# Kernel tuning notes

Measured on AMD Instinct MI355X. Metric: run time of the kernel, lower is better.

The kernel has to match this reference:

```python
import jax, jax.numpy as jnp
import numpy as np

N, D, H = 1024, 256, 512


def _linear_init(key, fan_in, fan_out):
    kw, kb = jax.random.split(key)
    bound = 1.0 / np.sqrt(fan_in)
    w = jax.random.uniform(kw, (fan_in, fan_out), jnp.float32, -bound, bound)
    b = jax.random.uniform(kb, (fan_out,), jnp.float32, -bound, bound)
    return w, b


def setup_inputs() -> dict:
    key = jax.random.key(0)
    ks = jax.random.split(key, 8)
    domain_a = jax.random.normal(ks[0], (N, D), jnp.float32)
    domain_b = jax.random.normal(ks[1], (N, D), jnp.float32)
    mu_w0, mu_b0 = _linear_init(ks[2], D, H)
    mu_w1, mu_b1 = _linear_init(ks[3], H, H)
    mu_w2, mu_b2 = _linear_init(ks[4], H, D)
    lv_w0, lv_b0 = _linear_init(ks[5], D, H)
    lv_w1, lv_b1 = _linear_init(ks[6], H, H)
    lv_w2, lv_b2 = _linear_init(ks[7], H, D)
    return dict(domain_a=domain_a, domain_b=domain_b,
                mu_w0=mu_w0, mu_b0=mu_b0, mu_w1=mu_w1, mu_b1=mu_b1, mu_w2=mu_w2, mu_b2=mu_b2,
                lv_w0=lv_w0, lv_b0=lv_b0, lv_w1=lv_w1, lv_b1=lv_b1, lv_w2=lv_w2, lv_b2=lv_b2)


def _net(x, ws, bs, final_act):
    h = x
    for i in range(len(ws)):
        h = h @ ws[i] + bs[i]
        if i < len(ws) - 1:
            h = jax.nn.relu(h)
    return final_act(h)


def _l2norm(h):
    # L2NormEncoder == F.normalize(dim=-1), eps clamp like torch
    n = jnp.maximum(jnp.linalg.norm(h, axis=-1, keepdims=True), 1e-12)
    return h / n


def reference(domain_a, domain_b, mu_w0, mu_b0, mu_w1, mu_b1, mu_w2, mu_b2,
              lv_w0, lv_b0, lv_w1, lv_b1, lv_w2, lv_b2):
    mu_ws, mu_bs = [mu_w0, mu_w1, mu_w2], [mu_b0, mu_b1, mu_b2]
    lv_ws, lv_bs = [lv_w0, lv_w1, lv_w2], [lv_b0, lv_b1, lv_b2]

    # ---- embedding-model loss: prob-model params frozen (requires_grad=False) ----
    sg = jax.lax.stop_gradient
    mu = _net(domain_a, [sg(w) for w in mu_ws], [sg(b) for b in mu_bs], _l2norm)
    log_var = _net(domain_a, [sg(w) for w in lv_ws], [sg(b) for b in lv_bs], jnp.tanh)
    inv_var = jnp.exp(-log_var)                                  # [N, D]
    pos_probs = jnp.sum(-(domain_b - mu) ** 2 * inv_var - log_var, axis=-1)  # [N]
    # pairwise: [i, j, d] = b[j, d] - mu[i, d]; mean over j
    diff2_mean = jnp.mean((domain_b[None, :, :] - mu[:, None, :]) ** 2, axis=1)  # [N, D]
    neg_probs = jnp.sum(-diff2_mean * inv_var - log_var, axis=-1)  # [N]
    embed_model_loss = jnp.mean(pos_probs - neg_probs)

    # ---- prob-model loss: embeddings detached, params trainable ----
    a_d, b_d = sg(domain_a), sg(domain_b)
    mu2 = _net(a_d, mu_ws, mu_bs, _l2norm)
    lv2 = _net(a_d, lv_ws, lv_bs, jnp.tanh)
    prob_model_loss = jnp.mean(jnp.sum((b_d - mu2) ** 2 * jnp.exp(-lv2) + lv2, axis=-1))

    emb_coef, prob_coef = 1.0, 1.0
    loss = emb_coef * embed_model_loss + prob_coef * prob_model_loss
    return loss
```

## Files before the change

kernel.cpp:

```cpp
#include <hip/hip_runtime.h>
#include <hip/hip_fp16.h>

#define N_ROWS 1024
#define DIM 256
#define HID 512

typedef _Float16 half_t;
typedef __attribute__((ext_vector_type(8))) _Float16 half8v;
typedef __attribute__((ext_vector_type(16))) float f32x16;

struct Params {
    const float* a;
    const float* b;
    const float* w[6];
    const float* bias[6];
    unsigned* flags;
    float* acc;
    unsigned* done;
    float* ebsum;
    float* eb2sum;
    float* g_mu;
    half_t* wt[6];
    float* out;
};

__global__ __launch_bounds__(256) void prep_kernel(Params p) {
    const int y = blockIdx.y, bx = blockIdx.x, tid = threadIdx.x;

    if (y == 6) {
        if (bx >= 64) return;
        const int d = tid, r0 = bx * 16;
        float s = 0.f, s2 = 0.f;
        #pragma unroll
        for (int r = 0; r < 16; ++r) {
            float v = p.b[(r0 + r) * DIM + d];
            s += v; s2 = fmaf(v, v, s2);
        }
        atomicAdd(&p.ebsum[d], s);
        atomicAdd(&p.eb2sum[d], s2);
        return;
    }
    const float* src = p.w[y];
    half_t* dst = p.wt[y];
    const int K = (y < 2) ? DIM : HID;
    const int N = (y < 4) ? HID : DIM;
    const int C = K >> 5;
    const int ntiles = (K >> 5) * (N >> 5);
    if (bx >= ntiles) return;
    const int tilesN = N >> 5;
    const int tk = bx / tilesN, tn = bx % tilesN;
    const int r = tid >> 3, c4 = (tid & 7) * 4;
    float4 v = *(const float4*)&src[(tk * 32 + r) * N + tn * 32 + c4];
    const int which = r >> 4, hi = (r >> 3) & 1, e = r & 7;
    half_t* base = dst + ((tn * C + tk) * 2 + which) * 512 + hi * 256 + e;
    base[(c4 + 0) * 8] = (half_t)v.x;
    base[(c4 + 1) * 8] = (half_t)v.y;
    base[(c4 + 2) * 8] = (half_t)v.z;
    base[(c4 + 3) * 8] = (half_t)v.w;
}

template <int NC, int NT, int MODE>
__device__ __forceinline__ void gemm_layer(const half_t* __restrict__ Xin,
                                           const half_t* __restrict__ Wfrag,
                                           const float* __restrict__ bias,
                                           half_t* __restrict__ Xout,
                                           float* __restrict__ rawL,
                                           float* __restrict__ gmu,
                                           const int R0) {
    const int tid = threadIdx.x;
    const int w = tid >> 6, lane = tid & 63;
    const int lr = lane & 31, hi = lane >> 5;
    const int sa = (lr >> 3) & 3;
    const int aoff0 = lr * 40 + ((hi ^ sa) * 8);
    const int aoff1 = lr * 40 + (((hi + 2) ^ sa) * 8);

    const half_t* Wp[NT];
    #pragma unroll
    for (int ct = 0; ct < NT; ++ct)
        Wp[ct] = Wfrag + (w * NT + ct) * NC * 1024 + lane * 8;

    f32x16 acc[NT];
    #pragma unroll
    for (int ct = 0; ct < NT; ++ct)
        #pragma unroll
        for (int i = 0; i < 16; ++i) acc[ct][i] = 0.f;

    half8v wbuf[NT][4][2], abuf[2][2];
    #define ISSUE_W(ct, c)                                                    \
        do {                                                                  \
            wbuf[ct][(c) & 3][0] = *(const half8v*)(Wp[ct] + (c) * 1024);     \
            wbuf[ct][(c) & 3][1] = *(const half8v*)(Wp[ct] + (c) * 1024 + 512);\
        } while (0)
    #define ISSUE_A(c)                                                        \
        do {                                                                  \
            abuf[(c) & 1][0] = *(const half8v*)&Xin[(c) * 1280 + aoff0];      \
            abuf[(c) & 1][1] = *(const half8v*)&Xin[(c) * 1280 + aoff1];      \
        } while (0)

    #pragma unroll
    for (int c = 0; c < 4 && c < NC; ++c) {
        #pragma unroll
        for (int ct = 0; ct < NT; ++ct) ISSUE_W(ct, c);
    }
    ISSUE_A(0);
    if (NC > 1) ISSUE_A(1);

    #pragma unroll
    for (int c = 0; c < NC; ++c) {
        half8v av0 = abuf[c & 1][0], av1 = abuf[c & 1][1];
        if (c + 2 < NC) ISSUE_A(c + 2);
        #pragma unroll
        for (int ct = 0; ct < NT; ++ct) {
            half8v bv0 = wbuf[ct][c & 3][0], bv1 = wbuf[ct][c & 3][1];
            if (c + 4 < NC) ISSUE_W(ct, c + 4);
            acc[ct] = __builtin_amdgcn_mfma_f32_32x32x16_f16(av0, bv0, acc[ct], 0, 0, 0);
            acc[ct] = __builtin_amdgcn_mfma_f32_32x32x16_f16(av1, bv1, acc[ct], 0, 0, 0);
        }
    }
    #undef ISSUE_W
    #undef ISSUE_A

    #pragma unroll
    for (int ct = 0; ct < NT; ++ct) {
        const int col0 = (w * NT + ct) * 32;
        const int col = col0 + lr;
        const float bv = bias[col];
        #pragma unroll
        for (int r = 0; r < 16; ++r) {
            const int row = (r & 3) + 8 * (r >> 2) + 4 * hi;
            float v = acc[ct][r] + bv;
            if (MODE == 0) {
                v = fmaxf(v, 0.f);
                const int kbp = (lr >> 3) ^ ((row >> 3) & 3);
                Xout[(col0 >> 5) * 1280 + row * 40 + kbp * 8 + (lr & 7)] = (half_t)v;
            } else if (MODE == 1) {
                __hip_atomic_store(&gmu[(R0 + row) * DIM + col], v,
                                   __ATOMIC_RELAXED, __HIP_MEMORY_SCOPE_AGENT);
            } else {
                rawL[row * 256 + col] = v;
            }
        }
    }
}

__global__ void __launch_bounds__(512) main_kernel(Params p) {
    __shared__ alignas(16) char smem[81984];
    half_t* XA = (half_t*)smem;
    half_t* XB = (half_t*)(smem + 40960);
    float* rawL = (float*)(smem + 40960);
    float* bsum = (float*)(smem + 81920);

    const int bid = blockIdx.x, tid = threadIdx.x;
    const int net = bid & 1, g = bid >> 1, R0 = g * 32;

    {
        const int r = tid >> 4, q = tid & 15;
        const float* src = &p.a[(R0 + r) * DIM + q * 16];
        float4 v0 = *(const float4*)(src);
        float4 v1 = *(const float4*)(src + 4);
        float4 v2 = *(const float4*)(src + 8);
        float4 v3 = *(const float4*)(src + 12);
        half8v h0, h1;
        h0[0] = (half_t)v0.x; h0[1] = (half_t)v0.y; h0[2] = (half_t)v0.z; h0[3] = (half_t)v0.w;
        h0[4] = (half_t)v1.x; h0[5] = (half_t)v1.y; h0[6] = (half_t)v1.z; h0[7] = (half_t)v1.w;
        h1[0] = (half_t)v2.x; h1[1] = (half_t)v2.y; h1[2] = (half_t)v2.z; h1[3] = (half_t)v2.w;
        h1[4] = (half_t)v3.x; h1[5] = (half_t)v3.y; h1[6] = (half_t)v3.z; h1[7] = (half_t)v3.w;
        const int c = q >> 1, kb0 = (q & 1) * 2, s = (r >> 3) & 3;
        *(half8v*)&XA[c * 1280 + r * 40 + ((kb0 ^ s) * 8)] = h0;
        *(half8v*)&XA[c * 1280 + r * 40 + (((kb0 + 1) ^ s) * 8)] = h1;
    }
    __syncthreads();

    gemm_layer<8, 2, 0>(XA, p.wt[net], p.bias[net], XB, nullptr, nullptr, R0);
    __syncthreads();
    gemm_layer<16, 2, 0>(XB, p.wt[2 + net], p.bias[2 + net], XA, nullptr, nullptr, R0);
    __syncthreads();

    if (net == 0) {
        gemm_layer<16, 1, 1>(XA, p.wt[4], p.bias[4], nullptr, nullptr, p.g_mu, R0);
        asm volatile("s_waitcnt vmcnt(0)" ::: "memory");
        __syncthreads();
        if (tid == 0)
            __hip_atomic_store(&p.flags[g], 1u, __ATOMIC_RELAXED, __HIP_MEMORY_SCOPE_AGENT);
        return;
    }

    gemm_layer<16, 1, 2>(XA, p.wt[5], p.bias[5], nullptr, rawL, nullptr, R0);
    if (tid == 0) *bsum = 0.f;
    if (tid == 0) {
        while (__hip_atomic_load(&p.flags[g], __ATOMIC_RELAXED, __HIP_MEMORY_SCOPE_AGENT) == 0u)
            __builtin_amdgcn_s_sleep(1);
    }
    __syncthreads();
    asm volatile("" ::: "memory");

    const int wave = tid >> 6, lane = tid & 63;
    const float invN = 1.0f / (float)N_ROWS;
    float ebv[4], eb2v[4];
    #pragma unroll
    for (int t = 0; t < 4; ++t) {
        const int d = lane + t * 64;
        ebv[t]  = p.ebsum[d] * invN;
        eb2v[t] = p.eb2sum[d] * invN;
    }
    float wacc = 0.f;
    #pragma unroll
    for (int rr = 0; rr < 4; ++rr) {
        const int i = wave * 4 + rr;
        float m4[4], l4[4], ss = 0.f;
        #pragma unroll
        for (int t = 0; t < 4; ++t) {
            const int d = lane + t * 64;
            m4[t] = p.g_mu[(R0 + i) * DIM + d];
            l4[t] = rawL[i * 256 + d];
            ss = fmaf(m4[t], m4[t], ss);
        }
        #pragma unroll
        for (int o = 32; o > 0; o >>= 1) ss += __shfl_xor(ss, o, 64);
        const float inv_norm = 1.f / fmaxf(sqrtf(ss), 1e-12f);
        #pragma unroll
        for (int t = 0; t < 4; ++t) {
            float mu = m4[t] * inv_norm;
            float lv = tanhf(l4[t]);
            float iv = expf(-lv);
            float diff2 = fmaf(mu, mu, fmaf(-2.f * mu, ebv[t], eb2v[t]));
            wacc += fmaf(diff2, iv, lv);
        }
    }
    #pragma unroll
    for (int o = 32; o > 0; o >>= 1) wacc += __shfl_xor(wacc, o, 64);
    if (lane == 0) atomicAdd(bsum, wacc);
    __syncthreads();
    if (tid == 0) {
        atomicAdd(p.acc, *bsum);
        asm volatile("s_waitcnt vmcnt(0)" ::: "memory");
        unsigned prev = __hip_atomic_fetch_add(p.done, 1u, __ATOMIC_RELAXED,
                                               __HIP_MEMORY_SCOPE_AGENT);
        if (prev == 31u) {
            float v = __hip_atomic_load(p.acc, __ATOMIC_RELAXED, __HIP_MEMORY_SCOPE_AGENT);
            p.out[0] = v * (1.0f / (float)N_ROWS);
        }
    }
}

extern "C" void kernel_launch(void* const* d_in, const int* in_sizes, int n_in,
                              void* d_out, int out_size, void* d_ws, size_t ws_size,
                              hipStream_t stream) {
    Params p;
    p.a = (const float*)d_in[0];
    p.b = (const float*)d_in[1];
    p.w[0] = (const float*)d_in[2];  p.bias[0] = (const float*)d_in[3];
    p.w[2] = (const float*)d_in[4];  p.bias[2] = (const float*)d_in[5];
    p.w[4] = (const float*)d_in[6];  p.bias[4] = (const float*)d_in[7];
    p.w[1] = (const float*)d_in[8];  p.bias[1] = (const float*)d_in[9];
    p.w[3] = (const float*)d_in[10]; p.bias[3] = (const float*)d_in[11];
    p.w[5] = (const float*)d_in[12]; p.bias[5] = (const float*)d_in[13];

    float* f = (float*)d_ws;
    p.flags  = (unsigned*)f;
    p.acc    = f + 32;
    p.done   = (unsigned*)(f + 33);
    p.ebsum  = f + 64;
    p.eb2sum = f + 320;
    p.g_mu   = f + 1024;
    half_t* hb = (half_t*)(p.g_mu + N_ROWS * DIM);
    p.wt[0] = hb;  hb += HID * DIM;
    p.wt[1] = hb;  hb += HID * DIM;
    p.wt[2] = hb;  hb += HID * HID;
    p.wt[3] = hb;  hb += HID * HID;
    p.wt[4] = hb;  hb += DIM * HID;
    p.wt[5] = hb;  hb += DIM * HID;
    p.out   = (float*)d_out;

    hipMemsetAsync(d_ws, 0, 4096, stream);
    prep_kernel<<<dim3(256, 7), 256, 0, stream>>>(p);
    main_kernel<<<64, 512, 0, stream>>>(p);
}
```

Measured before the change: 35.18 us.

## Transpose weights via LDS, deepen weight prefetch, store mu exchange in fp16

The weight-prep kernel now stages each 32x32 tile in shared memory and writes MFMA fragments as contiguous 4-half vectors instead of scattered 2-byte stores. The GEMM weight prefetch depth goes from 4 to 6 chunks to hide more global-load latency, at the cost of more registers. The cross-block mu buffer is stored and loaded as fp16 rather than fp32, which halves that traffic but lowers the precision of mu before normalization.

```diff
diff --git a/kernel.cpp b/kernel.cpp
--- a/kernel.cpp
+++ b/kernel.cpp
@@ -6,6 +6,7 @@
 #define HID 512
 
 typedef _Float16 half_t;
+typedef __attribute__((ext_vector_type(4))) _Float16 half4v;
 typedef __attribute__((ext_vector_type(8))) _Float16 half8v;
 typedef __attribute__((ext_vector_type(16))) float f32x16;
 
@@ -19,7 +20,7 @@
     unsigned* done;
     float* ebsum;
     float* eb2sum;
-    float* g_mu;
+    unsigned short* g_mu;
     half_t* wt[6];
     float* out;
 };
@@ -40,23 +41,34 @@
         atomicAdd(&p.eb2sum[d], s2);
         return;
     }
+    __shared__ float T[32][33];
     const float* src = p.w[y];
     half_t* dst = p.wt[y];
     const int K = (y < 2) ? DIM : HID;
     const int N = (y < 4) ? HID : DIM;
     const int C = K >> 5;
-    const int ntiles = (K >> 5) * (N >> 5);
-    if (bx >= ntiles) return;
     const int tilesN = N >> 5;
+    if (bx >= C * tilesN) return;
     const int tk = bx / tilesN, tn = bx % tilesN;
-    const int r = tid >> 3, c4 = (tid & 7) * 4;
-    float4 v = *(const float4*)&src[(tk * 32 + r) * N + tn * 32 + c4];
-    const int which = r >> 4, hi = (r >> 3) & 1, e = r & 7;
-    half_t* base = dst + ((tn * C + tk) * 2 + which) * 512 + hi * 256 + e;
-    base[(c4 + 0) * 8] = (half_t)v.x;
-    base[(c4 + 1) * 8] = (half_t)v.y;
-    base[(c4 + 2) * 8] = (half_t)v.z;
-    base[(c4 + 3) * 8] = (half_t)v.w;
+
+    {
+        const int r = tid >> 3, c4 = (tid & 7) * 4;
+        float4 v = *(const float4*)&src[(tk * 32 + r) * N + tn * 32 + c4];
+        T[r][c4 + 0] = v.x; T[r][c4 + 1] = v.y; T[r][c4 + 2] = v.z; T[r][c4 + 3] = v.w;
+    }
+    __syncthreads();
+
+    const int which = tid >> 7;
+    const int lane64 = (tid >> 1) & 63;
+    const int epart = tid & 1;
+    const int hi = lane64 >> 5, lr = lane64 & 31;
+    const int rbase = which * 16 + hi * 8 + epart * 4;
+    half4v h;
+    h[0] = (half_t)T[rbase + 0][lr];
+    h[1] = (half_t)T[rbase + 1][lr];
+    h[2] = (half_t)T[rbase + 2][lr];
+    h[3] = (half_t)T[rbase + 3][lr];
+    *(half4v*)&dst[((tn * C + tk) * 2 + which) * 512 + lane64 * 8 + epart * 4] = h;
 }
 
 template <int NC, int NT, int MODE>
@@ -65,7 +77,7 @@
                                            const float* __restrict__ bias,
                                            half_t* __restrict__ Xout,
                                            float* __restrict__ rawL,
-                                           float* __restrict__ gmu,
+                                           unsigned short* __restrict__ gmu,
                                            const int R0) {
     const int tid = threadIdx.x;
     const int w = tid >> 6, lane = tid & 63;
@@ -73,6 +85,7 @@
     const int sa = (lr >> 3) & 3;
     const int aoff0 = lr * 40 + ((hi ^ sa) * 8);
     const int aoff1 = lr * 40 + (((hi + 2) ^ sa) * 8);
+    constexpr int PFW = (NC < 6) ? NC : 6;
 
     const half_t* Wp[NT];
     #pragma unroll
@@ -85,20 +98,20 @@
         #pragma unroll
         for (int i = 0; i < 16; ++i) acc[ct][i] = 0.f;
 
-    half8v wbuf[NT][4][2], abuf[2][2];
-    #define ISSUE_W(ct, c)                                                    \
-        do {                                                                  \
-            wbuf[ct][(c) & 3][0] = *(const half8v*)(Wp[ct] + (c) * 1024);     \
-            wbuf[ct][(c) & 3][1] = *(const half8v*)(Wp[ct] + (c) * 1024 + 512);\
+    half8v wbuf[NT][6][2], abuf[2][2];
+    #define ISSUE_W(ct, c)                                                     \
+        do {                                                                   \
+            wbuf[ct][(c) % 6][0] = *(const half8v*)(Wp[ct] + (c) * 1024);      \
+            wbuf[ct][(c) % 6][1] = *(const half8v*)(Wp[ct] + (c) * 1024 + 512);\
         } while (0)
-    #define ISSUE_A(c)                                                        \
-        do {                                                                  \
-            abuf[(c) & 1][0] = *(const half8v*)&Xin[(c) * 1280 + aoff0];      \
-            abuf[(c) & 1][1] = *(const half8v*)&Xin[(c) * 1280 + aoff1];      \
+    #define ISSUE_A(c)                                                         \
+        do {                                                                   \
+            abuf[(c) & 1][0] = *(const half8v*)&Xin[(c) * 1280 + aoff0];       \
+            abuf[(c) & 1][1] = *(const half8v*)&Xin[(c) * 1280 + aoff1];       \
         } while (0)
 
     #pragma unroll
-    for (int c = 0; c < 4 && c < NC; ++c) {
+    for (int c = 0; c < PFW; ++c) {
         #pragma unroll
         for (int ct = 0; ct < NT; ++ct) ISSUE_W(ct, c);
     }
@@ -111,8 +124,8 @@
         if (c + 2 < NC) ISSUE_A(c + 2);
         #pragma unroll
         for (int ct = 0; ct < NT; ++ct) {
-            half8v bv0 = wbuf[ct][c & 3][0], bv1 = wbuf[ct][c & 3][1];
-            if (c + 4 < NC) ISSUE_W(ct, c + 4);
+            half8v bv0 = wbuf[ct][c % 6][0], bv1 = wbuf[ct][c % 6][1];
+            if (c + PFW < NC) ISSUE_W(ct, c + PFW);
             acc[ct] = __builtin_amdgcn_mfma_f32_32x32x16_f16(av0, bv0, acc[ct], 0, 0, 0);
             acc[ct] = __builtin_amdgcn_mfma_f32_32x32x16_f16(av1, bv1, acc[ct], 0, 0, 0);
         }
@@ -134,7 +147,9 @@
                 const int kbp = (lr >> 3) ^ ((row >> 3) & 3);
                 Xout[(col0 >> 5) * 1280 + row * 40 + kbp * 8 + (lr & 7)] = (half_t)v;
             } else if (MODE == 1) {
-                __hip_atomic_store(&gmu[(R0 + row) * DIM + col], v,
+                union { half_t h; unsigned short u; } cv;
+                cv.h = (half_t)v;
+                __hip_atomic_store(&gmu[(R0 + row) * DIM + col], cv.u,
                                    __ATOMIC_RELAXED, __HIP_MEMORY_SCOPE_AGENT);
             } else {
                 rawL[row * 256 + col] = v;
@@ -211,7 +226,11 @@
         #pragma unroll
         for (int t = 0; t < 4; ++t) {
             const int d = lane + t * 64;
-            m4[t] = p.g_mu[(R0 + i) * DIM + d];
+            unsigned short mu_u = __hip_atomic_load(&p.g_mu[(R0 + i) * DIM + d],
+                                                    __ATOMIC_RELAXED, __HIP_MEMORY_SCOPE_AGENT);
+            union { unsigned short u; half_t h; } cv;
+            cv.u = mu_u;
+            m4[t] = (float)cv.h;
             l4[t] = rawL[i * 256 + d];
             ss = fmaf(m4[t], m4[t], ss);
         }
@@ -262,7 +281,7 @@
     p.done   = (unsigned*)(f + 33);
     p.ebsum  = f + 64;
     p.eb2sum = f + 320;
-    p.g_mu   = f + 1024;
+    p.g_mu   = (unsigned short*)(f + 1024);
     half_t* hb = (half_t*)(p.g_mu + N_ROWS * DIM);
     p.wt[0] = hb;  hb += HID * DIM;
     p.wt[1] = hb;  hb += HID * DIM;
```

New measurement: 33.90 us. -3.6%, faster.
